# Performance work log

Measured on AMD Instinct MI355X. Metric: run time of the kernel, lower is better.

The kernel has to match this reference:

```python
import jax, jax.numpy as jnp
import numpy as np

N_GENE, N_CT, N_REF, N_SAMPLE = 50000, 64, 16, 1024

def setup_inputs() -> dict:
    key = jax.random.key(0)
    k1, k2, k3, k4, k5, k6 = jax.random.split(key, 6)
    x = jax.random.normal(k1, (N_GENE * N_CT * N_REF,), dtype=jnp.float32)
    idx = jax.random.randint(k2, (N_CT, N_GENE), 0, N_CT * N_GENE)
    # RefCombLayer weight: uniform around 1/n_ref
    num = 1.0 / N_REF
    w_ref = jax.random.uniform(k3, (N_REF * N_CT,), minval=num - num / 5, maxval=num + num / 5, dtype=jnp.float32)
    # CelltypeScaleLayer weight: normal(1.0, 0.1)
    w_ct = 1.0 + 0.1 * jax.random.normal(k4, (N_CT,), dtype=jnp.float32)
    # StretchLayer weight: normal(1.0, 0.1)
    w_stretch = 1.0 + 0.1 * jax.random.normal(k5, (N_GENE,), dtype=jnp.float32)
    # conv1 kernel: (n_sample, 1, n_kernel), normal(1/n_ct, 0.25/n_ct)
    conv_w = (1.0 / N_CT) + (0.25 / N_CT) * jax.random.normal(k6, (N_SAMPLE, 1, N_CT), dtype=jnp.float32)
    return {"x": x, "idx": idx, "w_ref": w_ref, "w_ct": w_ct,
            "w_stretch": w_stretch, "conv_w": conv_w,
            "N_batch": 1, "N_feature": N_GENE * N_CT}


def reference(x, idx, w_ref, w_ct, w_stretch, conv_w, N_batch, N_feature):
    # RefCombLayer: elementwise mul by per-gene-tiled ref weights
    y = x * jnp.tile(w_ref, N_GENE)                       # [n_gene*n_ct*n_ref]
    # SliceSumLayer: sum over n_ref slices
    y0 = y.reshape(N_CT * N_GENE, N_REF).sum(axis=1)      # [n_ct*n_gene]
    # CelltypeScaleLayer: gather per cell type, scale, flatten transposed
    z = y0[idx] * w_ct[:, None]                           # [n_ct, n_gene]
    y1 = z.T.reshape(-1)                                  # [n_gene*n_ct], gene-major
    # StretchLayer: per-gene weight repeated n_ct times
    y2 = y1 * jnp.repeat(w_stretch, N_CT)                 # [n_gene*n_ct]
    # Conv1d(1, n_sample, kernel=n_ct, stride=n_ct) == per-gene dot with kernel
    yk = y2.reshape(N_GENE, N_CT)                         # [n_gene, n_ct]
    out = jnp.einsum('gk,sk->sg', yk, conv_w[:, 0, :])    # [n_sample, n_gene]
    return (out, y0, y1, y2)
```

## Files before the change

### kernel.cpp

```cpp
#include <hip/hip_runtime.h>

#define NG 50000
#define NCT 64
#define NREF 16
#define NS 1024
#define N0 (NCT * NG)

#define OFF_Y0 ((size_t)NS * NG)
#define OFF_Y1 (OFF_Y0 + N0)
#define OFF_Y2 (OFF_Y1 + N0)

typedef __attribute__((ext_vector_type(8))) short bf16x8;
typedef __attribute__((ext_vector_type(4))) float f32x4;

__device__ __forceinline__ unsigned short f2bf(float f) {
    union { float f; unsigned u; } v; v.f = f;
    unsigned r = v.u + 0x7fff + ((v.u >> 16) & 1);
    return (unsigned short)(r >> 16);
}
__device__ __forceinline__ float bf2f(unsigned short b) {
    union { float f; unsigned u; } v; v.u = ((unsigned)b) << 16;
    return v.f;
}

__global__ __launch_bounds__(256) void k_y0(const float* __restrict__ x,
                                            const float* __restrict__ w_ref,
                                            float* __restrict__ y0) {
    __shared__ f32x4 wl[256];
    const int tid = threadIdx.x;
    wl[tid] = reinterpret_cast<const f32x4*>(w_ref)[tid];
    __syncthreads();
    const int row = tid & 63;
    const f32x4 w0 = wl[row * 4 + 0];
    const f32x4 w1 = wl[row * 4 + 1];
    const f32x4 w2 = wl[row * 4 + 2];
    const f32x4 w3 = wl[row * 4 + 3];
    const f32x4* x4 = reinterpret_cast<const f32x4*>(x);
    const size_t stride = (size_t)gridDim.x * 256;
    for (size_t j = (size_t)blockIdx.x * 256 + tid; j < (size_t)N0; j += stride) {
        const f32x4* xp = x4 + j * 4;
        f32x4 a = __builtin_nontemporal_load(xp + 0);
        f32x4 b = __builtin_nontemporal_load(xp + 1);
        f32x4 c = __builtin_nontemporal_load(xp + 2);
        f32x4 d = __builtin_nontemporal_load(xp + 3);
        float s = a.x * w0.x + a.y * w0.y + a.z * w0.z + a.w * w0.w
                + b.x * w1.x + b.y * w1.y + b.z * w1.z + b.w * w1.w
                + c.x * w2.x + c.y * w2.y + c.z * w2.z + c.w * w2.w
                + d.x * w3.x + d.y * w3.y + d.z * w3.z + d.w * w3.w;
        y0[j] = s;
    }
}

__global__ __launch_bounds__(512) void k_pc(const float* __restrict__ y0,
                                            const int* __restrict__ idx,
                                            const float* __restrict__ w_ct,
                                            const float* __restrict__ w_stretch,
                                            const float* __restrict__ cw,
                                            float* __restrict__ y1,
                                            float* __restrict__ y2,
                                            float* __restrict__ out) {
    __shared__ float T[4][64 * 9];
    __shared__ unsigned short Phi[2][32 * 72];
    __shared__ unsigned short Plo[2][32 * 72];

    const int tid  = threadIdx.x;
    const int lane = tid & 63;
    const int wid  = tid >> 6;
    const int g0   = blockIdx.x * 64;

    if (wid < 4) {
        const int p = wid;
        const float wct = w_ct[lane];
        float* Tp = T[p];
        for (int h = 0; h < 2; ++h) {
            const int gbase = g0 + 32 * h + p * 8;
            int iids[8];
#pragma unroll
            for (int k = 0; k < 8; ++k) {
                int j = lane & 7;
                int c = (lane >> 3) + k * 8;
                int g = min(gbase + j, NG - 1);
                iids[k] = idx[c * NG + g];
            }
            float vals[8];
#pragma unroll
            for (int k = 0; k < 8; ++k) vals[k] = y0[iids[k]];
#pragma unroll
            for (int k = 0; k < 8; ++k) {
                int j = lane & 7;
                int c = (lane >> 3) + k * 8;
                Tp[c * 9 + j] = vals[k];
            }
#pragma unroll
            for (int j = 0; j < 8; ++j) {
                int g = gbase + j;
                float t = Tp[lane * 9 + j];
                float v1 = t * wct;
                float v2 = v1 * w_stretch[min(g, NG - 1)];
                int base = (p * 8 + j) * 72 + lane;
                unsigned short hh = f2bf(v2);
                Phi[h][base] = hh;
                Plo[h][base] = f2bf(v2 - bf2f(hh));
                if (g < NG) {
                    size_t o = (size_t)g * 64 + lane;
                    __builtin_nontemporal_store(v1, y1 + o);
                    __builtin_nontemporal_store(v2, y2 + o);
                }
            }
            __syncthreads();
        }
    } else {
        const int cwv = wid - 4;
        const int l15 = lane & 15;
        const int l4  = lane >> 4;
        __syncthreads();
        for (int h = 0; h < 2; ++h) {
            bf16x8 Ah[2][2], Al[2][2];
#pragma unroll
            for (int m = 0; m < 2; ++m) {
                int grow = m * 16 + l15;
#pragma unroll
                for (int ks = 0; ks < 2; ++ks) {
                    int koff = ks * 32 + l4 * 8;
                    Ah[m][ks] = *reinterpret_cast<const bf16x8*>(&Phi[h][grow * 72 + koff]);
                    Al[m][ks] = *reinterpret_cast<const bf16x8*>(&Plo[h][grow * 72 + koff]);
                }
            }
            const int gh = g0 + 32 * h;
            for (int s0 = 0; s0 < NS; s0 += 128) {
                f32x4 acc[2][2];
#pragma unroll
                for (int m = 0; m < 2; ++m)
#pragma unroll
                    for (int n = 0; n < 2; ++n) acc[m][n] = (f32x4){0.f, 0.f, 0.f, 0.f};
#pragma unroll
                for (int n = 0; n < 2; ++n) {
                    const size_t srow = (size_t)(s0 + cwv * 32 + n * 16 + l15) * 64;
                    bf16x8 Bh[2], Bl[2];
#pragma unroll
                    for (int ks = 0; ks < 2; ++ks) {
                        int koff = ks * 32 + l4 * 8;
                        f32x4 va = *reinterpret_cast<const f32x4*>(cw + srow + koff);
                        f32x4 vb = *reinterpret_cast<const f32x4*>(cw + srow + koff + 4);
#pragma unroll
                        for (int e = 0; e < 4; ++e) {
                            unsigned short hv = f2bf(va[e]);
                            Bh[ks][e] = (short)hv;
                            Bl[ks][e] = (short)f2bf(va[e] - bf2f(hv));
                            hv = f2bf(vb[e]);
                            Bh[ks][e + 4] = (short)hv;
                            Bl[ks][e + 4] = (short)f2bf(vb[e] - bf2f(hv));
                        }
                    }
#pragma unroll
                    for (int m = 0; m < 2; ++m)
#pragma unroll
                        for (int ks = 0; ks < 2; ++ks) {
                            acc[m][n] = __builtin_amdgcn_mfma_f32_16x16x32_bf16(Ah[m][ks], Bh[ks], acc[m][n], 0, 0, 0);
                            acc[m][n] = __builtin_amdgcn_mfma_f32_16x16x32_bf16(Ah[m][ks], Bl[ks], acc[m][n], 0, 0, 0);
                            acc[m][n] = __builtin_amdgcn_mfma_f32_16x16x32_bf16(Al[m][ks], Bh[ks], acc[m][n], 0, 0, 0);
                        }
                }
#pragma unroll
                for (int m = 0; m < 2; ++m) {
                    int g4 = gh + m * 16 + l4 * 4;
                    if (g4 < NG) {
#pragma unroll
                        for (int n = 0; n < 2; ++n) {
                            int s = s0 + cwv * 32 + n * 16 + l15;
                            __builtin_nontemporal_store(acc[m][n], reinterpret_cast<f32x4*>(out + (size_t)s * NG + g4));
                        }
                    }
                }
            }
            if (h == 0) __syncthreads();
        }
    }
}

extern "C" void kernel_launch(void* const* d_in, const int* in_sizes, int n_in,
                              void* d_out, int out_size, void* d_ws, size_t ws_size,
                              hipStream_t stream) {
    const float* x         = (const float*)d_in[0];
    const int*   idx       = (const int*)d_in[1];
    const float* w_ref     = (const float*)d_in[2];
    const float* w_ct      = (const float*)d_in[3];
    const float* w_stretch = (const float*)d_in[4];
    const float* conv_w    = (const float*)d_in[5];

    float* out = (float*)d_out;
    float* y0  = out + OFF_Y0;
    float* y1  = out + OFF_Y1;
    float* y2  = out + OFF_Y2;

    k_y0<<<2048, 256, 0, stream>>>(x, w_ref, y0);
    k_pc<<<(NG + 63) / 64, 512, 0, stream>>>(y0, idx, w_ct, w_stretch, conv_w, y1, y2, out);
}
```

Baseline: 185.4 us.

## Precompute bf16 hi/lo split of conv weights and partition y0 gathers by quadrant

Adds a small kernel that converts conv_w once into bf16 hi/lo arrays in workspace, so the MFMA waves load pre-split operands instead of redoing the fp32-to-bf16 split for every sample tile in every block. It also makes the idx loads nontemporal and splits the y0 gather into four passes by index range, so concurrent gathers hit a narrower address window and may reuse L2 better. The cost is an extra kernel launch, a workspace dependency with a fallback path, and repeated branch checks in the gather loop.

```diff
diff --git a/kernel.cpp b/kernel.cpp
--- a/kernel.cpp
+++ b/kernel.cpp
@@ -5,6 +5,8 @@
 #define NREF 16
 #define NS 1024
 #define N0 (NCT * NG)
+#define NQ 4
+#define QSZ (N0 / NQ)
 
 #define OFF_Y0 ((size_t)NS * NG)
 #define OFF_Y1 (OFF_Y0 + N0)
@@ -12,6 +14,7 @@
 
 typedef __attribute__((ext_vector_type(8))) short bf16x8;
 typedef __attribute__((ext_vector_type(4))) float f32x4;
+typedef __attribute__((ext_vector_type(4))) unsigned short u16x4;
 
 __device__ __forceinline__ unsigned short f2bf(float f) {
     union { float f; unsigned u; } v; v.f = f;
@@ -51,11 +54,30 @@
     }
 }
 
+__global__ __launch_bounds__(256) void k_cw(const float* __restrict__ cw,
+                                            unsigned short* __restrict__ cwhi,
+                                            unsigned short* __restrict__ cwlo) {
+    int i = (blockIdx.x * 256 + threadIdx.x) * 4;
+    f32x4 v = *reinterpret_cast<const f32x4*>(cw + i);
+    u16x4 h, l;
+#pragma unroll
+    for (int e = 0; e < 4; ++e) {
+        unsigned short hh = f2bf(v[e]);
+        h[e] = hh;
+        l[e] = f2bf(v[e] - bf2f(hh));
+    }
+    *reinterpret_cast<u16x4*>(cwhi + i) = h;
+    *reinterpret_cast<u16x4*>(cwlo + i) = l;
+}
+
+template<bool PRECONV>
 __global__ __launch_bounds__(512) void k_pc(const float* __restrict__ y0,
                                             const int* __restrict__ idx,
                                             const float* __restrict__ w_ct,
                                             const float* __restrict__ w_stretch,
                                             const float* __restrict__ cw,
+                                            const unsigned short* __restrict__ cwhi,
+                                            const unsigned short* __restrict__ cwlo,
                                             float* __restrict__ y1,
                                             float* __restrict__ y2,
                                             float* __restrict__ out) {
@@ -80,11 +102,19 @@
                 int j = lane & 7;
                 int c = (lane >> 3) + k * 8;
                 int g = min(gbase + j, NG - 1);
-                iids[k] = idx[c * NG + g];
+                iids[k] = __builtin_nontemporal_load(idx + c * NG + g);
             }
             float vals[8];
 #pragma unroll
-            for (int k = 0; k < 8; ++k) vals[k] = y0[iids[k]];
+            for (int k = 0; k < 8; ++k) vals[k] = 0.f;
+            for (int q = 0; q < NQ; ++q) {
+                const int lo = q * QSZ;
+#pragma unroll
+                for (int k = 0; k < 8; ++k) {
+                    if ((unsigned)(iids[k] - lo) < (unsigned)QSZ)
+                        vals[k] = y0[iids[k]];
+                }
+            }
 #pragma unroll
             for (int k = 0; k < 8; ++k) {
                 int j = lane & 7;
@@ -140,16 +170,21 @@
 #pragma unroll
                     for (int ks = 0; ks < 2; ++ks) {
                         int koff = ks * 32 + l4 * 8;
-                        f32x4 va = *reinterpret_cast<const f32x4*>(cw + srow + koff);
-                        f32x4 vb = *reinterpret_cast<const f32x4*>(cw + srow + koff + 4);
-#pragma unroll
-                        for (int e = 0; e < 4; ++e) {
-                            unsigned short hv = f2bf(va[e]);
-                            Bh[ks][e] = (short)hv;
-                            Bl[ks][e] = (short)f2bf(va[e] - bf2f(hv));
-                            hv = f2bf(vb[e]);
-                            Bh[ks][e + 4] = (short)hv;
-                            Bl[ks][e + 4] = (short)f2bf(vb[e] - bf2f(hv));
+                        if (PRECONV) {
+                            Bh[ks] = *reinterpret_cast<const bf16x8*>(cwhi + srow + koff);
+                            Bl[ks] = *reinterpret_cast<const bf16x8*>(cwlo + srow + koff);
+                        } else {
+                            f32x4 va = *reinterpret_cast<const f32x4*>(cw + srow + koff);
+                            f32x4 vb = *reinterpret_cast<const f32x4*>(cw + srow + koff + 4);
+#pragma unroll
+                            for (int e = 0; e < 4; ++e) {
+                                unsigned short hv = f2bf(va[e]);
+                                Bh[ks][e] = (short)hv;
+                                Bl[ks][e] = (short)f2bf(va[e] - bf2f(hv));
+                                hv = f2bf(vb[e]);
+                                Bh[ks][e + 4] = (short)hv;
+                                Bl[ks][e + 4] = (short)f2bf(vb[e] - bf2f(hv));
+                            }
                         }
                     }
 #pragma unroll
@@ -194,5 +229,18 @@
     float* y2  = out + OFF_Y2;
 
     k_y0<<<2048, 256, 0, stream>>>(x, w_ref, y0);
-    k_pc<<<(NG + 63) / 64, 512, 0, stream>>>(y0, idx, w_ct, w_stretch, conv_w, y1, y2, out);
-}
+
+    const size_t need = 2 * (size_t)NS * NCT * sizeof(unsigned short);
+    if (ws_size >= need) {
+        unsigned short* cwhi = (unsigned short*)d_ws;
+        unsigned short* cwlo = cwhi + (size_t)NS * NCT;
+        k_cw<<<NS * NCT / 1024, 256, 0, stream>>>(conv_w, cwhi, cwlo);
+        k_pc<true><<<(NG + 63) / 64, 512, 0, stream>>>(y0, idx, w_ct, w_stretch, conv_w,
+                                                       cwhi, cwlo, y1, y2, out);
+    } else {
+        k_pc<false><<<(NG + 63) / 64, 512, 0, stream>>>(y0, idx, w_ct, w_stretch, conv_w,
+                                                        (const unsigned short*)nullptr,
+                                                        (const unsigned short*)nullptr,
+                                                        y1, y2, out);
+    }
+}
```

After: 190.6 us. 2.8% more time.

## Recompute gathered y0 values from x inside k_pc to remove dependency

Applied to the files above, without the earlier changes.

The projection kernel no longer reads y0. For each gathered index it loads the 16 x values directly and computes the weighted ref sum itself, using w_ref staged in shared memory. This removes the ordering dependency on k_y0, so k_y0 is launched after k_pc and only writes the y0 output. The cost is that the gather now reads 64 bytes of x per element instead of 4 bytes of y0, which adds heavy random traffic. The idx loads are also made nontemporal.

```diff
diff --git a/kernel.cpp b/kernel.cpp
--- a/kernel.cpp
+++ b/kernel.cpp
@@ -51,7 +51,8 @@
     }
 }
 
-__global__ __launch_bounds__(512) void k_pc(const float* __restrict__ y0,
+__global__ __launch_bounds__(512) void k_pc(const float* __restrict__ x,
+                                            const float* __restrict__ w_ref,
                                             const int* __restrict__ idx,
                                             const float* __restrict__ w_ct,
                                             const float* __restrict__ w_stretch,
@@ -59,6 +60,7 @@
                                             float* __restrict__ y1,
                                             float* __restrict__ y2,
                                             float* __restrict__ out) {
+    __shared__ f32x4 wl[256];
     __shared__ float T[4][64 * 9];
     __shared__ unsigned short Phi[2][32 * 72];
     __shared__ unsigned short Plo[2][32 * 72];
@@ -67,6 +69,11 @@
     const int lane = tid & 63;
     const int wid  = tid >> 6;
     const int g0   = blockIdx.x * 64;
+
+    if (tid < 256) wl[tid] = reinterpret_cast<const f32x4*>(w_ref)[tid];
+    __syncthreads();
+
+    const f32x4* x4 = reinterpret_cast<const f32x4*>(x);
 
     if (wid < 4) {
         const int p = wid;
@@ -80,11 +87,33 @@
                 int j = lane & 7;
                 int c = (lane >> 3) + k * 8;
                 int g = min(gbase + j, NG - 1);
-                iids[k] = idx[c * NG + g];
+                iids[k] = __builtin_nontemporal_load(idx + c * NG + g);
             }
             float vals[8];
 #pragma unroll
-            for (int k = 0; k < 8; ++k) vals[k] = y0[iids[k]];
+            for (int sb = 0; sb < 2; ++sb) {
+                f32x4 xd[4][4];
+#pragma unroll
+                for (int e = 0; e < 4; ++e) {
+                    const f32x4* xp = x4 + (size_t)iids[sb * 4 + e] * 4;
+                    xd[e][0] = __builtin_nontemporal_load(xp + 0);
+                    xd[e][1] = __builtin_nontemporal_load(xp + 1);
+                    xd[e][2] = __builtin_nontemporal_load(xp + 2);
+                    xd[e][3] = __builtin_nontemporal_load(xp + 3);
+                }
+#pragma unroll
+                for (int e = 0; e < 4; ++e) {
+                    int row = iids[sb * 4 + e] & 63;
+                    float s = 0.f;
+#pragma unroll
+                    for (int q = 0; q < 4; ++q) {
+                        f32x4 w = wl[row * 4 + q];
+                        f32x4 v = xd[e][q];
+                        s += v.x * w.x + v.y * w.y + v.z * w.z + v.w * w.w;
+                    }
+                    vals[sb * 4 + e] = s;
+                }
+            }
 #pragma unroll
             for (int k = 0; k < 8; ++k) {
                 int j = lane & 7;
@@ -193,6 +222,7 @@
     float* y1  = out + OFF_Y1;
     float* y2  = out + OFF_Y2;
 
+    k_pc<<<(NG + 63) / 64, 512, 0, stream>>>(x, w_ref, idx, w_ct, w_stretch,
+                                             conv_w, y1, y2, out);
     k_y0<<<2048, 256, 0, stream>>>(x, w_ref, y0);
-    k_pc<<<(NG + 63) / 64, 512, 0, stream>>>(y0, idx, w_ct, w_stretch, conv_w, y1, y2, out);
-}
+}
```

Result: slower. 354.3 us (+91.1%).
